# Performance work log

Measured on AMD Instinct MI355X. Metric: run time of the kernel, lower is better.

The kernel has to match this reference:

```python
import jax, jax.numpy as jnp
import numpy as np


def setup_inputs() -> dict:
    key = jax.random.key(0)
    ks = jax.random.split(key, 5)
    B, T, C, H, E = 8, 2048, 1024, 2048, 8
    n_layer = 12
    x = jax.random.normal(ks[0], (B, T, C), dtype=jnp.float32)
    w_router = jax.random.normal(ks[1], (C, E), dtype=jnp.float32) * 0.02
    w_c_fc = jax.random.normal(ks[2], (E, C, H), dtype=jnp.float32) * 0.02
    w_gate = jax.random.normal(ks[3], (E, C, H), dtype=jnp.float32) * 0.02
    w_c_proj = jax.random.normal(ks[4], (E, H, C), dtype=jnp.float32) * (0.02 * (2 * n_layer) ** -0.5)
    return {
        "x": x, "w_router": w_router, "w_c_fc": w_c_fc,
        "w_gate": w_gate, "w_c_proj": w_c_proj,
        "top_k": 2, "n_experts": E, "expert_capacity": 640,
    }


def reference(x, w_router, w_c_fc, w_gate, w_c_proj, top_k, n_experts, expert_capacity):
    B, T, C = x.shape
    # ---- router ----
    gate_logits = jnp.einsum('btc,ce->bte', x, w_router)
    gate_probs = jax.nn.softmax(gate_logits, axis=-1)  # (B,T,E)

    # ---- per-batch top-k dispatch (cumsum slot assignment + scatter) ----
    def dispatch(xb, pb):
        # xb: (T,C), pb: (T,E)
        topk_p, topk_i = jax.lax.top_k(pb, top_k)              # (T,k)
        ei = jnp.swapaxes(topk_i, 0, 1).ravel()                # (k*T,) k-major
        oh = jax.nn.one_hot(ei, n_experts, dtype=jnp.int32)    # (k*T,E)
        pos = jnp.cumsum(oh, axis=0) * oh - 1                  # slot within expert
        pos = jnp.swapaxes(pos.reshape(top_k, T, n_experts), 0, 1).max(axis=2)  # (T,k)
        ei = jnp.swapaxes(ei.reshape(top_k, T), 0, 1)          # (T,k)
        buf = jnp.zeros((n_experts, expert_capacity, C), dtype=xb.dtype)
        xr = jnp.repeat(xb, top_k, axis=0)                     # (T*k,C) token-major
        buf = buf.at[ei.ravel(), pos.ravel()].set(xr)          # overflow slots dropped
        return topk_p, pos, ei, buf

    topk_p, pos, ei, buf = jax.vmap(dispatch)(x, gate_probs)   # buf: (B,E,cap,C)

    # ---- batched expert SwiGLU GEMMs ----
    ein = jnp.swapaxes(buf, 0, 1).reshape(n_experts, B * expert_capacity, C)
    h = jnp.einsum('eti,eih->eth', ein, w_c_fc)
    g = jax.nn.silu(jnp.einsum('eti,eih->eth', ein, w_gate))
    o = jnp.einsum('eth,eho->eto', g * h, w_c_proj)
    eo = jnp.swapaxes(o.reshape(n_experts, B, expert_capacity, C), 0, 1)  # (B,E,cap,C)

    # ---- weighted combine gather ----
    def combine(eo_b, i_b, p_b, pr_b):
        sel = eo_b[i_b, p_b]                                   # (T,k,C)
        return jnp.sum(pr_b[..., None] * sel, axis=1)          # (T,C)

    y = jax.vmap(combine)(eo, ei, pos, topk_p)                 # (B,T,C)
    return y
```

## Files before the change

kernel.cpp:

```cpp
#include <hip/hip_runtime.h>
#include <stdint.h>

#define B_   8
#define T_   2048
#define C_   1024
#define H_   2048
#define E_   8
#define CAP_ 640
#define RPE_ (B_*CAP_)
#define BT_  (B_*T_)
#define NE_  2

typedef __attribute__((ext_vector_type(8))) short bf16x8;
typedef __attribute__((ext_vector_type(4))) float f32x4;

static __device__ __forceinline__ unsigned short f2bf(float f){
  union { float f; uint32_t u; } a; a.f = f;
  uint32_t u = a.u;
  uint32_t r = (u + 0x7FFFu + ((u >> 16) & 1u)) >> 16;
  return (unsigned short)r;
}

#define GLD16(gp, lp) __builtin_amdgcn_global_load_lds( \
    (__attribute__((address_space(1))) void*)(gp), \
    (__attribute__((address_space(3))) void*)(lp), 16, 0, 0)

__global__ __launch_bounds__(256) void router_kernel(
    const float* __restrict__ x, const float* __restrict__ wr,
    unsigned short* __restrict__ xbf, float* __restrict__ probs2, int* __restrict__ idx2)
{
  int bt = blockIdx.x;
  int tid = threadIdx.x;
  const float4 v = ((const float4*)(x + (size_t)bt*C_))[tid];
  ushort4 u;
  u.x = f2bf(v.x); u.y = f2bf(v.y); u.z = f2bf(v.z); u.w = f2bf(v.w);
  ((ushort4*)(xbf + (size_t)bt*C_))[tid] = u;

  double p[8];
  #pragma unroll
  for (int e=0;e<8;e++) p[e]=0.0;
  const float xv[4] = {v.x, v.y, v.z, v.w};
  #pragma unroll
  for (int j=0;j<4;j++){
    int c = tid*4+j;
    const float* wrow = wr + c*8;
    #pragma unroll
    for (int e=0;e<8;e++) p[e] += (double)xv[j] * (double)wrow[e];
  }
  __shared__ double red[8][256];
  #pragma unroll
  for (int e=0;e<8;e++) red[e][tid] = p[e];
  __syncthreads();
  for (int s=128; s>0; s>>=1){
    if (tid < s){
      #pragma unroll
      for (int e=0;e<8;e++) red[e][tid] += red[e][tid+s];
    }
    __syncthreads();
  }
  if (tid==0){
    double lg[8];
    #pragma unroll
    for (int e=0;e<8;e++) lg[e]=red[e][0];
    double mx = lg[0];
    #pragma unroll
    for (int e=1;e<8;e++) if (lg[e]>mx) mx=lg[e];
    double s=0.0, ex[8];
    #pragma unroll
    for (int e=0;e<8;e++){ ex[e]=exp(lg[e]-mx); s+=ex[e]; }
    int i1=0; double b1=ex[0];
    #pragma unroll
    for (int e=1;e<8;e++) if (ex[e]>b1){ b1=ex[e]; i1=e; }
    int i2=-1; double b2=-1.0;
    #pragma unroll
    for (int e=0;e<8;e++) if (e!=i1 && ex[e]>b2){ b2=ex[e]; i2=e; }
    probs2[bt*2+0] = (float)(b1/s);
    probs2[bt*2+1] = (float)(b2/s);
    idx2[bt*2+0] = i1;
    idx2[bt*2+1] = i2;
  }
}

__global__ __launch_bounds__(256) void transp_fcg_kernel(
    const float* __restrict__ fc, const float* __restrict__ gate,
    unsigned short* __restrict__ dst)
{
  __shared__ float t[32][33];
  int e = blockIdx.z;
  int n0 = blockIdx.x*32, k0 = blockIdx.y*32;
  int tx = threadIdx.x & 31, ty = threadIdx.x >> 5;
  #pragma unroll
  for (int sel=0; sel<2; ++sel){
    const float* s = (sel ? gate : fc) + ((size_t)e*C_ + k0)*H_ + n0;
    #pragma unroll
    for (int i=0;i<32;i+=8) t[ty+i][tx] = s[(size_t)(ty+i)*H_ + tx];
    __syncthreads();
    #pragma unroll
    for (int i=0;i<32;i+=8){
      int jj = ty+i;
      int drow = n0*2 + ((jj & 16) << 1) + sel*16 + (jj & 15);
      dst[((size_t)e*4096 + drow)*1024 + k0 + tx] = f2bf(t[tx][jj]);
    }
    __syncthreads();
  }
}

__global__ __launch_bounds__(256) void transp_kernel(
    const float* __restrict__ src, unsigned short* __restrict__ dst, int K, int N)
{
  __shared__ float t[32][33];
  int e = blockIdx.z;
  int n0 = blockIdx.x*32, k0 = blockIdx.y*32;
  int tx = threadIdx.x & 31, ty = threadIdx.x >> 5;
  const float* s = src + ((size_t)e*K + k0)*N + n0;
  #pragma unroll
  for (int i=0;i<32;i+=8) t[ty+i][tx] = s[(size_t)(ty+i)*N + tx];
  __syncthreads();
  unsigned short* d = dst + ((size_t)e*N + n0)*K + k0;
  #pragma unroll
  for (int i=0;i<32;i+=8) d[(size_t)(ty+i)*K + tx] = f2bf(t[tx][ty+i]);
}

__global__ void scan_kernel(const int* __restrict__ idx2, int* __restrict__ pos, int* __restrict__ cnt)
{
  int b = blockIdx.x, lane = threadIdx.x;
  unsigned long long below = (lane == 0) ? 0ull : (~0ull >> (64 - lane));
  int base = 0;
  for (int k=0;k<2;k++){
    for (int c0=0;c0<T_;c0+=64){
      int t = c0 + lane;
      int e = idx2[((b*T_ + t)<<1) + k];
      unsigned long long mym = 0; int addv = 0;
      #pragma unroll
      for (int ee=0; ee<8; ++ee){
        unsigned long long m = __ballot(e == ee);
        if (ee == e) mym = m;
        if (lane == ee) addv = __popcll(m);
      }
      int mybase = __shfl(base, e, 64);
      pos[((b*T_+t)<<1)+k] = mybase + __popcll(mym & below);
      base += addv;
    }
  }
  if (lane < 8) cnt[b*8 + lane] = (base < CAP_) ? base : CAP_;
}

__global__ void offsets_kernel(const int* __restrict__ cnt, int* __restrict__ off, int* __restrict__ Me)
{
  int e = threadIdx.x;
  if (e < 8){
    int s = 0;
    for (int b=0;b<8;b++){ off[e*8+b] = s; s += cnt[b*8+e]; }
    Me[e] = s;
  }
}

__global__ void fill_kernel(const int* __restrict__ idx2, const int* __restrict__ pos,
                            const int* __restrict__ off, const float* __restrict__ probs2,
                            int* __restrict__ token_src, float* __restrict__ row_prob)
{
  int a = blockIdx.x*256 + threadIdx.x;
  if (a >= BT_*2) return;
  int bt = a >> 1, k = a & 1;
  int b = bt >> 11;
  int e = idx2[bt*2+k];
  int p = pos[bt*2+k];
  if (p < CAP_){
    int r = e*RPE_ + off[e*8+b] + p;
    token_src[r] = bt;
    row_prob[r] = probs2[bt*2+k];
  }
}

__global__ __launch_bounds__(256) void gemm1_kernel(
    const unsigned short* __restrict__ xbf,
    const unsigned short* __restrict__ wifcg,
    const int* __restrict__ token_src,
    const int* __restrict__ Me,
    unsigned short* __restrict__ act,
    int e0)
{
  const int ez = blockIdx.z, e = e0 + ez, mt = blockIdx.y, nt = blockIdx.x;
  const int M = Me[e];
  if (mt*128 >= M) return;

  __shared__ __align__(16) unsigned char lds[2][32768];

  const int tid = threadIdx.x;
  const int w = tid >> 6, l = tid & 63;
  const int wrow = w >> 1, wcol = w & 1;
  const int r8 = l >> 3;
  const unsigned swz16 = (unsigned)(((l & 7) ^ r8) * 16);

  unsigned offA[4], offB[4], ldsOff[4];
  #pragma unroll
  for (int j = 0; j < 4; ++j){
    int row = w*32 + j*8 + r8;
    int tok = token_src[e*RPE_ + mt*128 + row];
    offA[j]  = (unsigned)tok * 2048u + swz16;
    offB[j]  = (unsigned)(ez*4096 + nt*128 + row) * 2048u + swz16;
    ldsOff[j] = (unsigned)(w*32 + j*8) * 128u;
  }

  f32x4 acc[4][4];
  #pragma unroll
  for (int i=0;i<4;i++)
    #pragma unroll
    for (int j=0;j<4;j++) acc[i][j] = (f32x4){0.f,0.f,0.f,0.f};

  const unsigned char* gA = (const unsigned char*)xbf;
  const unsigned char* gB = (const unsigned char*)wifcg;

  auto stage = [&](int kt, int bb){
    const unsigned kb = (unsigned)kt * 128u;
    #pragma unroll
    for (int j=0;j<4;++j) GLD16(gA + offA[j] + kb, &lds[bb][0]     + ldsOff[j]);
    #pragma unroll
    for (int j=0;j<4;++j) GLD16(gB + offB[j] + kb, &lds[bb][16384] + ldsOff[j]);
  };
  auto compute = [&](int bb){
    #pragma unroll
    for (int kh=0; kh<2; ++kh){
      bf16x8 afr[4], bfr[4];
      #pragma unroll
      for (int fm=0; fm<4; ++fm){
        int row = wrow*64 + fm*16 + (l & 15);
        int gnum = kh*4 + (l >> 4);
        int byt = row*128 + ((gnum ^ (row & 7)) * 16);
        afr[fm] = *(const bf16x8*)(&lds[bb][0] + byt);
      }
      #pragma unroll
      for (int fn=0; fn<4; ++fn){
        int row = wcol*64 + fn*16 + (l & 15);
        int gnum = kh*4 + (l >> 4);
        int byt = row*128 + ((gnum ^ (row & 7)) * 16);
        bfr[fn] = *(const bf16x8*)(&lds[bb][16384] + byt);
      }
      #pragma unroll
      for (int fm=0; fm<4; ++fm)
        #pragma unroll
        for (int fn=0; fn<4; ++fn)
          acc[fm][fn] = __builtin_amdgcn_mfma_f32_16x16x32_bf16(afr[fm], bfr[fn], acc[fm][fn], 0,0,0);
    }
  };

  stage(0, 0);
  __syncthreads();
  for (int kt = 0; kt < 16; ++kt){
    if (kt+1 < 16) stage(kt+1, (kt+1)&1);
    compute(kt&1);
    __syncthreads();
  }

  #pragma unroll
  for (int fm=0; fm<4; ++fm){
    #pragma unroll
    for (int t=0; t<2; ++t){
      f32x4 h = acc[fm][2*t], g = acc[fm][2*t+1];
      #pragma unroll
      for (int r=0; r<4; ++r){
        int row = mt*128 + wrow*64 + fm*16 + (l>>4)*4 + r;
        int col = nt*64 + wcol*32 + t*16 + (l & 15);
        float gv = g[r];
        float a = (gv / (1.f + __expf(-gv))) * h[r];
        act[((size_t)ez*RPE_ + row)*(size_t)H_ + col] = f2bf(a);
      }
    }
  }
}

__global__ __launch_bounds__(256) void gemm2_kernel(
    const unsigned short* __restrict__ act,
    const unsigned short* __restrict__ wprojT,
    const int* __restrict__ token_src,
    const float* __restrict__ row_prob,
    const int* __restrict__ Me,
    float* __restrict__ y,
    int e0)
{
  const int ez = blockIdx.z, e = e0 + ez, mt = blockIdx.y, nt = blockIdx.x;
  const int M = Me[e];
  if (mt*128 >= M) return;

  __shared__ __align__(16) unsigned char lds[2][32768];

  const int tid = threadIdx.x;
  const int w = tid >> 6, l = tid & 63;
  const int wrow = w >> 1, wcol = w & 1;
  const int r8 = l >> 3;
  const unsigned swz16 = (unsigned)(((l & 7) ^ r8) * 16);

  unsigned offA[4], offB[4], ldsOff[4];
  #pragma unroll
  for (int j = 0; j < 4; ++j){
    int row = w*32 + j*8 + r8;
    offA[j] = (unsigned)(ez*RPE_ + mt*128 + row) * 4096u + swz16;
    offB[j] = (unsigned)(ez*C_ + nt*128 + row) * 4096u + swz16;
    ldsOff[j] = (unsigned)(w*32 + j*8) * 128u;
  }

  f32x4 acc[4][4];
  #pragma unroll
  for (int i=0;i<4;i++)
    #pragma unroll
    for (int j=0;j<4;j++) acc[i][j] = (f32x4){0.f,0.f,0.f,0.f};

  const unsigned char* gA = (const unsigned char*)act;
  const unsigned char* gB = (const unsigned char*)wprojT;

  auto stage = [&](int kt, int bb){
    const unsigned kb = (unsigned)kt * 128u;
    #pragma unroll
    for (int j=0;j<4;++j) GLD16(gA + offA[j] + kb, &lds[bb][0]     + ldsOff[j]);
    #pragma unroll
    for (int j=0;j<4;++j) GLD16(gB + offB[j] + kb, &lds[bb][16384] + ldsOff[j]);
  };
  auto compute = [&](int bb){
    #pragma unroll
    for (int kh=0; kh<2; ++kh){
      bf16x8 afr[4], bfr[4];
      #pragma unroll
      for (int fm=0; fm<4; ++fm){
        int row = wrow*64 + fm*16 + (l & 15);
        int gnum = kh*4 + (l >> 4);
        int byt = row*128 + ((gnum ^ (row & 7)) * 16);
        afr[fm] = *(const bf16x8*)(&lds[bb][0] + byt);
      }
      #pragma unroll
      for (int fn=0; fn<4; ++fn){
        int row = wcol*64 + fn*16 + (l & 15);
        int gnum = kh*4 + (l >> 4);
        int byt = row*128 + ((gnum ^ (row & 7)) * 16);
        bfr[fn] = *(const bf16x8*)(&lds[bb][16384] + byt);
      }
      #pragma unroll
      for (int fm=0; fm<4; ++fm)
        #pragma unroll
        for (int fn=0; fn<4; ++fn)
          acc[fm][fn] = __builtin_amdgcn_mfma_f32_16x16x32_bf16(afr[fm], bfr[fn], acc[fm][fn], 0,0,0);
    }
  };

  stage(0, 0);
  __syncthreads();
  for (int kt = 0; kt < 32; ++kt){
    if (kt+1 < 32) stage(kt+1, (kt+1)&1);
    compute(kt&1);
    __syncthreads();
  }

  #pragma unroll
  for (int fm=0; fm<4; ++fm){
    #pragma unroll
    for (int r=0; r<4; ++r){
      int rloc = mt*128 + wrow*64 + fm*16 + (l>>4)*4 + r;
      if (rloc < M){
        int bt  = token_src[e*RPE_ + rloc];
        float p = row_prob[e*RPE_ + rloc];
        float* yrow = y + (size_t)bt*C_;
        #pragma unroll
        for (int fn=0; fn<4; ++fn){
          int col = nt*128 + wcol*64 + fn*16 + (l & 15);
          atomicAdd(yrow + col, p * acc[fm][fn][r]);
        }
      }
    }
  }
}

extern "C" void kernel_launch(void* const* d_in, const int* in_sizes, int n_in,
                              void* d_out, int out_size, void* d_ws, size_t ws_size,
                              hipStream_t stream)
{
  const float* x   = (const float*)d_in[0];
  const float* wr  = (const float*)d_in[1];
  const float* wfc = (const float*)d_in[2];
  const float* wg  = (const float*)d_in[3];
  const float* wpj = (const float*)d_in[4];
  float* y = (float*)d_out;

  unsigned char* ws = (unsigned char*)d_ws;
  const size_t szXBF  = (size_t)BT_*C_*2;
  const size_t szFCGc = (size_t)NE_*4096*1024*2;
  const size_t szWPc  = (size_t)NE_*C_*H_*2;
  const size_t szFCGa = (size_t)E_*4096*1024*2;
  const size_t szWPa  = (size_t)E_*C_*H_*2;
  const size_t szACT  = (size_t)NE_*RPE_*H_*2;
  const size_t szMISC = 3*131072 + 2*(size_t)E_*RPE_*4 + 1024;

  const size_t need_small = szXBF + szFCGc + szWPc + szACT + szMISC;
  const size_t need_big   = szXBF + szFCGa + szWPa + szACT + szMISC;
  if (ws_size < need_small) return;
  const bool big = (ws_size >= need_big);

  const size_t szFCG = big ? szFCGa : szFCGc;
  const size_t szWP  = big ? szWPa  : szWPc;

  size_t oXBF = 0;
  size_t oFCG = oXBF + szXBF;
  size_t oWP  = oFCG + szFCG;
  size_t oACT = oWP  + szWP;
  size_t oM   = oACT + szACT;

  unsigned short* xbf    = (unsigned short*)(ws + oXBF);
  unsigned short* wifcg  = (unsigned short*)(ws + oFCG);
  unsigned short* wprojT = (unsigned short*)(ws + oWP);
  unsigned short* actc   = (unsigned short*)(ws + oACT);

  float* probs2    = (float*)(ws + oM);
  int*   idx2      = (int*)(ws + oM + 1*131072);
  int*   pos       = (int*)(ws + oM + 2*131072);
  int*   token_src = (int*)(ws + oM + 3*131072);
  float* row_prob  = (float*)(ws + oM + 3*131072 + (size_t)E_*RPE_*4);
  int*   cnt       = (int*)(ws + oM + 3*131072 + 2*(size_t)E_*RPE_*4);
  int*   off       = cnt + 64;
  int*   Me        = off + 64;

  hipMemsetAsync(y, 0, (size_t)out_size*4, stream);
  hipMemsetAsync(token_src, 0, (size_t)E_*RPE_*4, stream);

  router_kernel<<<BT_, 256, 0, stream>>>(x, wr, xbf, probs2, idx2);
  scan_kernel<<<B_, 64, 0, stream>>>(idx2, pos, cnt);
  offsets_kernel<<<1, 64, 0, stream>>>(cnt, off, Me);
  fill_kernel<<<(BT_*2+255)/256, 256, 0, stream>>>(idx2, pos, off, probs2, token_src, row_prob);

  if (big){
    transp_fcg_kernel<<<dim3(H_/32, C_/32, E_), 256, 0, stream>>>(wfc, wg, wifcg);
    transp_kernel<<<dim3(C_/32, H_/32, E_), 256, 0, stream>>>(wpj, wprojT, H_, C_);
  }

  for (int e0 = 0; e0 < E_; e0 += NE_){
    unsigned short* wfcg_c = wifcg;
    unsigned short* wpj_c  = wprojT;
    if (big){
      wfcg_c = wifcg  + (size_t)e0*4096*1024;
      wpj_c  = wprojT + (size_t)e0*C_*H_;
    } else {
      transp_fcg_kernel<<<dim3(H_/32, C_/32, NE_), 256, 0, stream>>>(
          wfc + (size_t)e0*C_*H_, wg + (size_t)e0*C_*H_, wifcg);
      transp_kernel<<<dim3(C_/32, H_/32, NE_), 256, 0, stream>>>(
          wpj + (size_t)e0*H_*C_, wprojT, H_, C_);
    }
    gemm1_kernel<<<dim3(4096/128, RPE_/128, NE_), 256, 0, stream>>>(
        xbf, wfcg_c, token_src, Me, actc, e0);
    gemm2_kernel<<<dim3(C_/128, RPE_/128, NE_), 256, 0, stream>>>(
        actc, wpj_c, token_src, row_prob, Me, y, e0);
  }
}
```

Before: 837.1 us.

## Switch expert GEMMs to a 4-stage LDS pipeline with explicit vmcnt waits

Both expert GEMM kernels drop the double-buffered 128-wide K tiles for 64-wide K tiles in a 4-slot ring, with three stages prefetched ahead. Explicit s_waitcnt vmcnt counts, raw s_barrier calls and sched_barrier fences replace __syncthreads. MFMA runs at raised wave priority via s_setprio, and the LDS swizzle is rebuilt for the 64-byte row layout. The deeper prefetch is meant to hide global-to-LDS latency. The cost is a barrier pair per smaller K step and hand-counted vmcnt values that must match the number of outstanding loads.

```diff
diff --git a/kernel.cpp b/kernel.cpp
--- a/kernel.cpp
+++ b/kernel.cpp
@@ -24,6 +24,19 @@
 #define GLD16(gp, lp) __builtin_amdgcn_global_load_lds( \
     (__attribute__((address_space(1))) void*)(gp), \
     (__attribute__((address_space(3))) void*)(lp), 16, 0, 0)
+
+#define SBAR0 __builtin_amdgcn_sched_barrier(0)
+
+#define PHASE(s, vm) do { \
+    asm volatile("s_waitcnt vmcnt(" #vm ")" ::: "memory"); \
+    SBAR0; \
+    __builtin_amdgcn_s_barrier(); \
+    SBAR0; \
+    COMPUTE(s); \
+    SBAR0; \
+    __builtin_amdgcn_s_barrier(); \
+    SBAR0; \
+  } while(0)
 
 __global__ __launch_bounds__(256) void router_kernel(
     const float* __restrict__ x, const float* __restrict__ wr,
@@ -184,84 +197,88 @@
   const int M = Me[e];
   if (mt*128 >= M) return;
 
-  __shared__ __align__(16) unsigned char lds[2][32768];
+  __shared__ __align__(16) unsigned char lds[65536];
 
   const int tid = threadIdx.x;
   const int w = tid >> 6, l = tid & 63;
   const int wrow = w >> 1, wcol = w & 1;
-  const int r8 = l >> 3;
-  const unsigned swz16 = (unsigned)(((l & 7) ^ r8) * 16);
-
-  unsigned offA[4], offB[4], ldsOff[4];
-  #pragma unroll
-  for (int j = 0; j < 4; ++j){
-    int row = w*32 + j*8 + r8;
-    int tok = token_src[e*RPE_ + mt*128 + row];
-    offA[j]  = (unsigned)tok * 2048u + swz16;
-    offB[j]  = (unsigned)(ez*4096 + nt*128 + row) * 2048u + swz16;
-    ldsOff[j] = (unsigned)(w*32 + j*8) * 128u;
-  }
-
-  f32x4 acc[4][4];
-  #pragma unroll
-  for (int i=0;i<4;i++)
-    #pragma unroll
-    for (int j=0;j<4;j++) acc[i][j] = (f32x4){0.f,0.f,0.f,0.f};
-
+
+  size_t aBase[2], bBase[2];
+  #pragma unroll
+  for (int j=0;j<2;++j){
+    int idx = j*256 + tid;
+    int r = idx >> 2, c = idx & 3;
+    int sc = c ^ ((r >> 1) & 3);
+    int tok = token_src[e*RPE_ + mt*128 + r];
+    aBase[j] = (size_t)tok*2048u + (unsigned)(sc*16);
+    bBase[j] = ((size_t)(ez*4096 + nt*128 + r))*2048u + (unsigned)(sc*16);
+  }
   const unsigned char* gA = (const unsigned char*)xbf;
   const unsigned char* gB = (const unsigned char*)wifcg;
 
-  auto stage = [&](int kt, int bb){
-    const unsigned kb = (unsigned)kt * 128u;
-    #pragma unroll
-    for (int j=0;j<4;++j) GLD16(gA + offA[j] + kb, &lds[bb][0]     + ldsOff[j]);
-    #pragma unroll
-    for (int j=0;j<4;++j) GLD16(gB + offB[j] + kb, &lds[bb][16384] + ldsOff[j]);
-  };
-  auto compute = [&](int bb){
-    #pragma unroll
-    for (int kh=0; kh<2; ++kh){
-      bf16x8 afr[4], bfr[4];
-      #pragma unroll
-      for (int fm=0; fm<4; ++fm){
-        int row = wrow*64 + fm*16 + (l & 15);
-        int gnum = kh*4 + (l >> 4);
-        int byt = row*128 + ((gnum ^ (row & 7)) * 16);
-        afr[fm] = *(const bf16x8*)(&lds[bb][0] + byt);
-      }
-      #pragma unroll
-      for (int fn=0; fn<4; ++fn){
-        int row = wcol*64 + fn*16 + (l & 15);
-        int gnum = kh*4 + (l >> 4);
-        int byt = row*128 + ((gnum ^ (row & 7)) * 16);
-        bfr[fn] = *(const bf16x8*)(&lds[bb][16384] + byt);
-      }
-      #pragma unroll
-      for (int fm=0; fm<4; ++fm)
-        #pragma unroll
-        for (int fn=0; fn<4; ++fn)
-          acc[fm][fn] = __builtin_amdgcn_mfma_f32_16x16x32_bf16(afr[fm], bfr[fn], acc[fm][fn], 0,0,0);
-    }
-  };
-
-  stage(0, 0);
-  __syncthreads();
-  for (int kt = 0; kt < 16; ++kt){
-    if (kt+1 < 16) stage(kt+1, (kt+1)&1);
-    compute(kt&1);
-    __syncthreads();
-  }
+  unsigned rdA[4], rdB[4];
+  const int g = l >> 4;
+  #pragma unroll
+  for (int f=0; f<4; ++f){
+    int ra = wrow*64 + f*16 + (l & 15);
+    rdA[f] = (unsigned)(ra*64 + ((g ^ ((ra>>1)&3)) << 4));
+    int rb = wcol*64 + f*16 + (l & 15);
+    rdB[f] = (unsigned)(32768 + rb*64 + ((g ^ ((rb>>1)&3)) << 4));
+  }
+
+  f32x4 acc[4][4];
+  #pragma unroll
+  for (int i=0;i<4;i++)
+    #pragma unroll
+    for (int j=0;j<4;j++) acc[i][j] = (f32x4){0.f,0.f,0.f,0.f};
+
+  #define STAGE(s) do { \
+    unsigned slot_ = ((unsigned)(s)&3u)*8192u; \
+    unsigned kb_ = (unsigned)(s)*64u; \
+    GLD16(gA + aBase[0] + kb_, lds + slot_ + 0*4096 + w*1024); \
+    GLD16(gA + aBase[1] + kb_, lds + slot_ + 1*4096 + w*1024); \
+    GLD16(gB + bBase[0] + kb_, lds + 32768 + slot_ + 0*4096 + w*1024); \
+    GLD16(gB + bBase[1] + kb_, lds + 32768 + slot_ + 1*4096 + w*1024); \
+  } while(0)
+
+  #define COMPUTE(s) do { \
+    unsigned slot_ = ((unsigned)(s)&3u)*8192u; \
+    bf16x8 afr[4], bfr[4]; \
+    _Pragma("unroll") \
+    for (int f=0; f<4; ++f) afr[f] = *(const bf16x8*)(lds + slot_ + rdA[f]); \
+    _Pragma("unroll") \
+    for (int f=0; f<4; ++f) bfr[f] = *(const bf16x8*)(lds + slot_ + rdB[f]); \
+    __builtin_amdgcn_s_setprio(1); \
+    _Pragma("unroll") \
+    for (int fm=0; fm<4; ++fm) \
+      _Pragma("unroll") \
+      for (int fn=0; fn<4; ++fn) \
+        acc[fm][fn] = __builtin_amdgcn_mfma_f32_16x16x32_bf16(afr[fm], bfr[fn], acc[fm][fn], 0,0,0); \
+    __builtin_amdgcn_s_setprio(0); \
+  } while(0)
+
+  STAGE(0); STAGE(1); STAGE(2);
+  for (int s = 0; s < 29; ++s){
+    STAGE(s+3);
+    PHASE(s, 12);
+  }
+  PHASE(29, 8);
+  PHASE(30, 4);
+  PHASE(31, 0);
+
+  #undef STAGE
+  #undef COMPUTE
 
   #pragma unroll
   for (int fm=0; fm<4; ++fm){
     #pragma unroll
     for (int t=0; t<2; ++t){
-      f32x4 h = acc[fm][2*t], g = acc[fm][2*t+1];
+      f32x4 h = acc[fm][2*t], gg = acc[fm][2*t+1];
       #pragma unroll
       for (int r=0; r<4; ++r){
         int row = mt*128 + wrow*64 + fm*16 + (l>>4)*4 + r;
         int col = nt*64 + wcol*32 + t*16 + (l & 15);
-        float gv = g[r];
+        float gv = gg[r];
         float a = (gv / (1.f + __expf(-gv))) * h[r];
         act[((size_t)ez*RPE_ + row)*(size_t)H_ + col] = f2bf(a);
       }
@@ -282,72 +299,76 @@
   const int M = Me[e];
   if (mt*128 >= M) return;
 
-  __shared__ __align__(16) unsigned char lds[2][32768];
+  __shared__ __align__(16) unsigned char lds[65536];
 
   const int tid = threadIdx.x;
   const int w = tid >> 6, l = tid & 63;
   const int wrow = w >> 1, wcol = w & 1;
-  const int r8 = l >> 3;
-  const unsigned swz16 = (unsigned)(((l & 7) ^ r8) * 16);
-
-  unsigned offA[4], offB[4], ldsOff[4];
-  #pragma unroll
-  for (int j = 0; j < 4; ++j){
-    int row = w*32 + j*8 + r8;
-    offA[j] = (unsigned)(ez*RPE_ + mt*128 + row) * 4096u + swz16;
-    offB[j] = (unsigned)(ez*C_ + nt*128 + row) * 4096u + swz16;
-    ldsOff[j] = (unsigned)(w*32 + j*8) * 128u;
-  }
-
-  f32x4 acc[4][4];
-  #pragma unroll
-  for (int i=0;i<4;i++)
-    #pragma unroll
-    for (int j=0;j<4;j++) acc[i][j] = (f32x4){0.f,0.f,0.f,0.f};
-
+
+  size_t aBase[2], bBase[2];
+  #pragma unroll
+  for (int j=0;j<2;++j){
+    int idx = j*256 + tid;
+    int r = idx >> 2, c = idx & 3;
+    int sc = c ^ ((r >> 1) & 3);
+    aBase[j] = ((size_t)(ez*RPE_ + mt*128 + r))*4096u + (unsigned)(sc*16);
+    bBase[j] = ((size_t)(ez*C_ + nt*128 + r))*4096u + (unsigned)(sc*16);
+  }
   const unsigned char* gA = (const unsigned char*)act;
   const unsigned char* gB = (const unsigned char*)wprojT;
 
-  auto stage = [&](int kt, int bb){
-    const unsigned kb = (unsigned)kt * 128u;
-    #pragma unroll
-    for (int j=0;j<4;++j) GLD16(gA + offA[j] + kb, &lds[bb][0]     + ldsOff[j]);
-    #pragma unroll
-    for (int j=0;j<4;++j) GLD16(gB + offB[j] + kb, &lds[bb][16384] + ldsOff[j]);
-  };
-  auto compute = [&](int bb){
-    #pragma unroll
-    for (int kh=0; kh<2; ++kh){
-      bf16x8 afr[4], bfr[4];
-      #pragma unroll
-      for (int fm=0; fm<4; ++fm){
-        int row = wrow*64 + fm*16 + (l & 15);
-        int gnum = kh*4 + (l >> 4);
-        int byt = row*128 + ((gnum ^ (row & 7)) * 16);
-        afr[fm] = *(const bf16x8*)(&lds[bb][0] + byt);
-      }
-      #pragma unroll
-      for (int fn=0; fn<4; ++fn){
-        int row = wcol*64 + fn*16 + (l & 15);
-        int gnum = kh*4 + (l >> 4);
-        int byt = row*128 + ((gnum ^ (row & 7)) * 16);
-        bfr[fn] = *(const bf16x8*)(&lds[bb][16384] + byt);
-      }
-      #pragma unroll
-      for (int fm=0; fm<4; ++fm)
-        #pragma unroll
-        for (int fn=0; fn<4; ++fn)
-          acc[fm][fn] = __builtin_amdgcn_mfma_f32_16x16x32_bf16(afr[fm], bfr[fn], acc[fm][fn], 0,0,0);
-    }
-  };
-
-  stage(0, 0);
-  __syncthreads();
-  for (int kt = 0; kt < 32; ++kt){
-    if (kt+1 < 32) stage(kt+1, (kt+1)&1);
-    compute(kt&1);
-    __syncthreads();
-  }
+  unsigned rdA[4], rdB[4];
+  const int g = l >> 4;
+  #pragma unroll
+  for (int f=0; f<4; ++f){
+    int ra = wrow*64 + f*16 + (l & 15);
+    rdA[f] = (unsigned)(ra*64 + ((g ^ ((ra>>1)&3)) << 4));
+    int rb = wcol*64 + f*16 + (l & 15);
+    rdB[f] = (unsigned)(32768 + rb*64 + ((g ^ ((rb>>1)&3)) << 4));
+  }
+
+  f32x4 acc[4][4];
+  #pragma unroll
+  for (int i=0;i<4;i++)
+    #pragma unroll
+    for (int j=0;j<4;j++) acc[i][j] = (f32x4){0.f,0.f,0.f,0.f};
+
+  #define STAGE(s) do { \
+    unsigned slot_ = ((unsigned)(s)&3u)*8192u; \
+    unsigned kb_ = (unsigned)(s)*64u; \
+    GLD16(gA + aBase[0] + kb_, lds + slot_ + 0*4096 + w*1024); \
+    GLD16(gA + aBase[1] + kb_, lds + slot_ + 1*4096 + w*1024); \
+    GLD16(gB + bBase[0] + kb_, lds + 32768 + slot_ + 0*4096 + w*1024); \
+    GLD16(gB + bBase[1] + kb_, lds + 32768 + slot_ + 1*4096 + w*1024); \
+  } while(0)
+
+  #define COMPUTE(s) do { \
+    unsigned slot_ = ((unsigned)(s)&3u)*8192u; \
+    bf16x8 afr[4], bfr[4]; \
+    _Pragma("unroll") \
+    for (int f=0; f<4; ++f) afr[f] = *(const bf16x8*)(lds + slot_ + rdA[f]); \
+    _Pragma("unroll") \
+    for (int f=0; f<4; ++f) bfr[f] = *(const bf16x8*)(lds + slot_ + rdB[f]); \
+    __builtin_amdgcn_s_setprio(1); \
+    _Pragma("unroll") \
+    for (int fm=0; fm<4; ++fm) \
+      _Pragma("unroll") \
+      for (int fn=0; fn<4; ++fn) \
+        acc[fm][fn] = __builtin_amdgcn_mfma_f32_16x16x32_bf16(afr[fm], bfr[fn], acc[fm][fn], 0,0,0); \
+    __builtin_amdgcn_s_setprio(0); \
+  } while(0)
+
+  STAGE(0); STAGE(1); STAGE(2);
+  for (int s = 0; s < 61; ++s){
+    STAGE(s+3);
+    PHASE(s, 12);
+  }
+  PHASE(61, 8);
+  PHASE(62, 4);
+  PHASE(63, 0);
+
+  #undef STAGE
+  #undef COMPUTE
 
   #pragma unroll
   for (int fm=0; fm<4; ++fm){
```

New measurement: 900.0 us. 1.08x slower.
